# Performance work log

Hardware: AMD Instinct MI355X
Metric: run time of the kernel (lower is better)

## Reference

```python
import jax, jax.numpy as jnp
import numpy as np

N, E, C, H = 50000, 600000, 128, 8
Dh = C // H  # 16
LN_EPS = 1e-5


def _ln(x, g, b):
    mu = jnp.mean(x, axis=-1, keepdims=True)
    var = jnp.var(x, axis=-1, keepdims=True)
    return (x - mu) * jax.lax.rsqrt(var + LN_EPS) * g + b


def setup_inputs() -> dict:
    key = jax.random.key(0)
    ks = jax.random.split(key, 20)
    s = lambda d: 1.0 / np.sqrt(d)
    inp = {
        "node_feats": jax.random.normal(ks[0], (N, C), jnp.float32),
        "edge_feats": jax.random.normal(ks[1], (E, C), jnp.float32),
        "coords": jax.random.normal(ks[2], (N, 3), jnp.float32),
        "edge_index": jax.random.randint(ks[3], (2, E), 0, N, jnp.int64),
        # attention projections (no bias since in==out channels)
        "Wq": jax.random.normal(ks[4], (C, C), jnp.float32) * s(C),
        "Wk": jax.random.normal(ks[5], (C, C), jnp.float32) * s(C),
        "Wv": jax.random.normal(ks[6], (C, C), jnp.float32) * s(C),
        "We": jax.random.normal(ks[7], (C + 1, C), jnp.float32) * s(C + 1),
        # output projections (with bias)
        "Wo_n": jax.random.normal(ks[8], (C, C), jnp.float32) * s(C),
        "bo_n": jnp.zeros((C,), jnp.float32),
        "Wo_e": jax.random.normal(ks[9], (C, C), jnp.float32) * s(C),
        "bo_e": jnp.zeros((C,), jnp.float32),
        # layer norms
        "ln1n_g": jnp.ones((C,), jnp.float32), "ln1n_b": jnp.zeros((C,), jnp.float32),
        "ln1e_g": jnp.ones((C,), jnp.float32), "ln1e_b": jnp.zeros((C,), jnp.float32),
        "ln2n_g": jnp.ones((C,), jnp.float32), "ln2n_b": jnp.zeros((C,), jnp.float32),
        "ln2e_g": jnp.ones((C,), jnp.float32), "ln2e_b": jnp.zeros((C,), jnp.float32),
        # FFN MLPs (bias-free)
        "Wn1": jax.random.normal(ks[10], (C, 2 * C), jnp.float32) * s(C),
        "Wn2": jax.random.normal(ks[11], (2 * C, C), jnp.float32) * s(2 * C),
        "We1": jax.random.normal(ks[12], (C, 2 * C), jnp.float32) * s(C),
        "We2": jax.random.normal(ks[13], (2 * C, C), jnp.float32) * s(2 * C),
    }
    return inp


def reference(node_feats, edge_feats, coords, edge_index,
              Wq, Wk, Wv, We, Wo_n, bo_n, Wo_e, bo_e,
              ln1n_g, ln1n_b, ln1e_g, ln1e_b,
              ln2n_g, ln2n_b, ln2e_g, ln2e_b,
              Wn1, Wn2, We1, We2):
    row, col = edge_index[0], edge_index[1]
    h_in1, e_in1 = node_feats, edge_feats

    h = _ln(node_feats, ln1n_g, ln1n_b)
    e = _ln(edge_feats, ln1e_g, ln1e_b)

    q = (h @ Wq).reshape(N, H, Dh)
    k = (h @ Wk).reshape(N, H, Dh)
    v = (h @ Wv).reshape(N, H, Dh)

    # edge feature: concat with 0.1 * pairwise distance
    d = coords[row] - coords[col]                                  # [E,3]
    dist = 0.1 * jnp.sqrt(jnp.sum(d * d, axis=-1, keepdims=True))  # [E,1]
    ep = (jnp.concatenate([e, dist], axis=-1) @ We).reshape(E, H, Dh)

    alpha = jnp.clip(k[row] * q[col] / np.sqrt(Dh), -5.0, 5.0) * ep  # [E,H,Dh]
    alphax = jnp.exp(jnp.clip(jnp.sum(alpha, axis=-1, keepdims=True), -5.0, 5.0))  # [E,H,1]

    wV = jax.ops.segment_sum(v[row] * alphax, col, num_segments=N)  # [N,H,Dh]
    z = jax.ops.segment_sum(alphax, col, num_segments=N)            # [N,H,1]

    h_attn = (wV / (z + 1e-6)).reshape(N, C)
    e_attn = alpha.reshape(E, C)

    h2 = h_in1 + (h_attn @ Wo_n + bo_n)
    e2 = e_in1 + (e_attn @ Wo_e + bo_e)

    hn = _ln(h2, ln2n_g, ln2n_b)
    en = _ln(e2, ln2e_g, ln2e_b)

    h3 = jax.nn.silu(hn @ Wn1) @ Wn2
    e3 = jax.nn.silu(en @ We1) @ We2

    return (h2 + h3, e2 + e3)
```

## Files before the change

kernel.cpp:

```cpp
#include <hip/hip_runtime.h>
#include <math.h>

#define NN 50000
#define NE 600000
#define C 128
#define H 8
#define LN_EPS 1e-5f

typedef __attribute__((ext_vector_type(8))) short bf16x8;
typedef __attribute__((ext_vector_type(4))) float f32x4;
#define MFMA16 __builtin_amdgcn_mfma_f32_16x16x32_bf16

__device__ __forceinline__ float clip5(float x){ return fminf(fmaxf(x, -5.f), 5.f); }

__device__ __forceinline__ float red32(float v){
  v += __shfl_xor(v, 1);  v += __shfl_xor(v, 2);  v += __shfl_xor(v, 4);
  v += __shfl_xor(v, 8);  v += __shfl_xor(v, 16);
  return v;
}

__device__ __forceinline__ unsigned short f2bf(float f){
  union { float f; unsigned u; } c; c.f = f;
  unsigned r = (c.u + 0x7fffu + ((c.u >> 16) & 1u)) >> 16;
  return (unsigned short)r;
}
__device__ __forceinline__ float bf2f(unsigned short u){
  union { unsigned u; float f; } c; c.u = ((unsigned)u) << 16;
  return c.f;
}

__device__ __forceinline__ bf16x8 ld_frag(const unsigned short* p){
  return *(const bf16x8*)p;
}

__global__ void __launch_bounds__(256)
k_node_ln_qkv(const float* __restrict__ nf,
              const float* __restrict__ Wq, const float* __restrict__ Wk,
              const float* __restrict__ Wv,
              const float* __restrict__ g, const float* __restrict__ b,
              float* __restrict__ qb, float* __restrict__ kb, float* __restrict__ vb)
{
  __shared__ __align__(16) float s_h[8][C];
  const int tid = threadIdx.x;
  const int slot = tid >> 5, tg = tid & 31, c0 = tg * 4;
  const int node = blockIdx.x * 8 + slot;
  const bool valid = node < NN;
  const size_t nn = valid ? (size_t)node : 0;

  const float4 x = *(const float4*)(nf + nn * C + c0);
  float s  = x.x + x.y + x.z + x.w;
  float sq = x.x*x.x + x.y*x.y + x.z*x.z + x.w*x.w;
  s = red32(s); sq = red32(sq);
  const float mu   = s * (1.0f / C);
  const float rstd = rsqrtf(sq * (1.0f / C) - mu * mu + LN_EPS);
  const float4 gg = *(const float4*)(g + c0);
  const float4 bb = *(const float4*)(b + c0);
  float4 hv;
  hv.x = (x.x - mu) * rstd * gg.x + bb.x;
  hv.y = (x.y - mu) * rstd * gg.y + bb.y;
  hv.z = (x.z - mu) * rstd * gg.z + bb.z;
  hv.w = (x.w - mu) * rstd * gg.w + bb.w;
  *(float4*)&s_h[slot][c0] = hv;
  __syncthreads();

  const float4* Wq4 = (const float4*)Wq;
  const float4* Wk4 = (const float4*)Wk;
  const float4* Wv4 = (const float4*)Wv;
  float aq0=0,aq1=0,aq2=0,aq3=0, ak0=0,ak1=0,ak2=0,ak3=0, av0=0,av1=0,av2=0,av3=0;
  #pragma unroll 8
  for (int k = 0; k < C; ++k){
    const float h = s_h[slot][k];
    const float4 wq = Wq4[k*32 + tg];
    const float4 wk = Wk4[k*32 + tg];
    const float4 wv = Wv4[k*32 + tg];
    aq0 += h*wq.x; aq1 += h*wq.y; aq2 += h*wq.z; aq3 += h*wq.w;
    ak0 += h*wk.x; ak1 += h*wk.y; ak2 += h*wk.z; ak3 += h*wk.w;
    av0 += h*wv.x; av1 += h*wv.y; av2 += h*wv.z; av3 += h*wv.w;
  }
  if (valid){
    float4 o;
    o.x=aq0; o.y=aq1; o.z=aq2; o.w=aq3; *(float4*)(qb + nn*C + c0) = o;
    o.x=ak0; o.y=ak1; o.z=ak2; o.w=ak3; *(float4*)(kb + nn*C + c0) = o;
    o.x=av0; o.y=av1; o.z=av2; o.w=av3; *(float4*)(vb + nn*C + c0) = o;
  }
}

__global__ void k_zero(float* __restrict__ p, size_t n){
  size_t i = (size_t)blockIdx.x * blockDim.x + threadIdx.x;
  const size_t st = (size_t)gridDim.x * blockDim.x;
  for (; i < n; i += st) p[i] = 0.f;
}

__global__ void __launch_bounds__(256)
k_prep(const float* __restrict__ Wn1, const float* __restrict__ Wn2,
       const float* __restrict__ We1, const float* __restrict__ We2,
       const float* __restrict__ We,  const float* __restrict__ Woe,
       unsigned short* __restrict__ o,
       unsigned short* __restrict__ weTh, unsigned short* __restrict__ weTl,
       unsigned short* __restrict__ woeTh, unsigned short* __restrict__ woeTl,
       float* __restrict__ we128f)
{
  const int id = blockIdx.x * 256 + threadIdx.x;
  if (id < 131072){
    const int w = id >> 15, e = id & 32767;
    const float* src; int K, Nn;
    if      (w == 0){ src = Wn1; K = 128; Nn = 256; }
    else if (w == 1){ src = Wn2; K = 256; Nn = 128; }
    else if (w == 2){ src = We1; K = 128; Nn = 256; }
    else            { src = We2; K = 256; Nn = 128; }
    const int n = (K == 128) ? (e >> 7) : (e >> 8);
    const int k = e - n * K;
    const float v = src[(size_t)k * Nn + n];
    const unsigned short h = f2bf(v);
    const unsigned short l = f2bf(v - bf2f(h));
    unsigned short* oh = o + (size_t)w * 65536;
    oh[e] = h;
    oh[32768 + e] = l;
  } else if (id < 147456){
    const int e = id - 131072;
    const int n = e >> 7, k = e & 127;
    const float v = We[(size_t)k * 128 + n];
    const unsigned short h = f2bf(v);
    weTh[e] = h; weTl[e] = f2bf(v - bf2f(h));
  } else if (id < 163840){
    const int e = id - 147456;
    const int n = e >> 7, k = e & 127;
    const float v = Woe[(size_t)k * 128 + n];
    const unsigned short h = f2bf(v);
    woeTh[e] = h; woeTl[e] = f2bf(v - bf2f(h));
  } else if (id < 163968){
    const int c = id - 163840;
    we128f[c] = We[128 * 128 + c];
  }
}

__global__ void __launch_bounds__(256, 2)
k_edge_mfma(const float* __restrict__ ef, const float* __restrict__ coords,
            const int* __restrict__ eidx,
            const float* __restrict__ qb, const float* __restrict__ kb,
            const float* __restrict__ vb,
            const unsigned short* __restrict__ weTh, const unsigned short* __restrict__ weTl,
            const float* __restrict__ we128,
            const unsigned short* __restrict__ woeTh, const unsigned short* __restrict__ woeTl,
            const float* __restrict__ boe,
            const float* __restrict__ g1, const float* __restrict__ b1,
            const float* __restrict__ g2, const float* __restrict__ b2,
            float* __restrict__ wV, float* __restrict__ zz,
            float* __restrict__ e2_out,
            unsigned short* __restrict__ enh, unsigned short* __restrict__ enl)
{
  const int tid  = threadIdx.x;
  const int wid  = tid >> 6;
  const int lane = tid & 63;
  const int r = lane & 15, q = lane >> 4;
  const int ebase = (blockIdx.x * 4 + wid) * 16;
  const int edge  = ebase + r;
  const size_t e128 = (size_t)edge * 128;

  float xv[32];
  #pragma unroll
  for (int gk = 0; gk < 4; ++gk){
    const float4 a = *(const float4*)(ef + e128 + gk*32 + q*8);
    const float4 b = *(const float4*)(ef + e128 + gk*32 + q*8 + 4);
    xv[gk*8+0]=a.x; xv[gk*8+1]=a.y; xv[gk*8+2]=a.z; xv[gk*8+3]=a.w;
    xv[gk*8+4]=b.x; xv[gk*8+5]=b.y; xv[gk*8+6]=b.z; xv[gk*8+7]=b.w;
  }
  float s = 0.f, sq = 0.f;
  #pragma unroll
  for (int j = 0; j < 32; ++j){ s += xv[j]; sq += xv[j]*xv[j]; }
  s  += __shfl_xor(s, 16);  s  += __shfl_xor(s, 32);
  sq += __shfl_xor(sq, 16); sq += __shfl_xor(sq, 32);
  const float mu   = s * (1.f/128.f);
  const float rstd = rsqrtf(sq * (1.f/128.f) - mu*mu + LN_EPS);

  bf16x8 bhf[4], blf[4];
  #pragma unroll
  for (int gk = 0; gk < 4; ++gk){
    const float4 ga = *(const float4*)(g1 + gk*32 + q*8);
    const float4 gb = *(const float4*)(g1 + gk*32 + q*8 + 4);
    const float4 ba = *(const float4*)(b1 + gk*32 + q*8);
    const float4 bb = *(const float4*)(b1 + gk*32 + q*8 + 4);
    const float gv[8] = {ga.x,ga.y,ga.z,ga.w,gb.x,gb.y,gb.z,gb.w};
    const float bv[8] = {ba.x,ba.y,ba.z,ba.w,bb.x,bb.y,bb.z,bb.w};
    union { unsigned short u[8]; bf16x8 v; } ph, pl;
    #pragma unroll
    for (int j = 0; j < 8; ++j){
      const float e = (xv[gk*8+j] - mu) * rstd * gv[j] + bv[j];
      ph.u[j] = f2bf(e);
      pl.u[j] = f2bf(e - bf2f(ph.u[j]));
    }
    bhf[gk] = ph.v; blf[gk] = pl.v;
  }

  const int row = eidx[edge];
  const int col = eidx[NE + edge];
  float dist;
  {
    const size_t r3 = (size_t)row*3, c3 = (size_t)col*3;
    const float dx = coords[r3+0]-coords[c3+0];
    const float dy = coords[r3+1]-coords[c3+1];
    const float dz = coords[r3+2]-coords[c3+2];
    dist = 0.1f * sqrtf(dx*dx + dy*dy + dz*dz);
  }

  const int src0 = (r + ((lane & 16) << 1)) << 2;
  const int src1 = src0 + 64;
  const bool hisel = (lane >= 32);

  f32x4 acc[8];
  #pragma unroll
  for (int nt = 0; nt < 8; ++nt) acc[nt] = (f32x4){0.f,0.f,0.f,0.f};

  #pragma unroll
  for (int w4 = 0; w4 < 4; ++w4){
    int tw[2][4];
    #pragma unroll
    for (int t = 0; t < 2; ++t){
      const int p = 2*w4 + t;
      f32x4 c = (f32x4){0.f,0.f,0.f,0.f};
      const size_t abase = (size_t)(p*16 + r) * 128 + q*8;
      #pragma unroll
      for (int gk = 0; gk < 4; ++gk){
        const bf16x8 ah = ld_frag(weTh + abase + gk*32);
        const bf16x8 al = ld_frag(weTl + abase + gk*32);
        c = MFMA16(ah, bhf[gk], c, 0, 0, 0);
        c = MFMA16(ah, blf[gk], c, 0, 0, 0);
        c = MFMA16(al, bhf[gk], c, 0, 0, 0);
      }
      const float4 w128 = *(const float4*)(we128 + p*16 + q*4);
      const float4 kr   = *(const float4*)(kb + (size_t)row*128 + p*16 + q*4);
      const float4 qc   = *(const float4*)(qb + (size_t)col*128 + p*16 + q*4);
      float al4[4];
      al4[0] = clip5(kr.x*qc.x*0.25f) * (c[0] + dist*w128.x);
      al4[1] = clip5(kr.y*qc.y*0.25f) * (c[1] + dist*w128.y);
      al4[2] = clip5(kr.z*qc.z*0.25f) * (c[2] + dist*w128.z);
      al4[3] = clip5(kr.w*qc.w*0.25f) * (c[3] + dist*w128.w);

      float hs = al4[0]+al4[1]+al4[2]+al4[3];
      hs += __shfl_xor(hs, 16); hs += __shfl_xor(hs, 32);
      const float ax = expf(clip5(hs));

      const float4 vr = *(const float4*)(vb + (size_t)row*128 + p*16 + q*4);
      const size_t wb = (size_t)col*128 + p*16 + q*4;
      atomicAdd(&wV[wb+0], vr.x*ax);
      atomicAdd(&wV[wb+1], vr.y*ax);
      atomicAdd(&wV[wb+2], vr.z*ax);
      atomicAdd(&wV[wb+3], vr.w*ax);
      if (q == 0) atomicAdd(&zz[(size_t)col*H + p], ax);

      unsigned short th[4], tl[4];
      #pragma unroll
      for (int i = 0; i < 4; ++i){
        th[i] = f2bf(al4[i]);
        tl[i] = f2bf(al4[i] - bf2f(th[i]));
      }
      tw[t][0] = (int)th[0] | ((int)th[1] << 16);
      tw[t][1] = (int)th[2] | ((int)th[3] << 16);
      tw[t][2] = (int)tl[0] | ((int)tl[1] << 16);
      tw[t][3] = (int)tl[2] | ((int)tl[3] << 16);
    }

    union { int i[4]; bf16x8 v; } a2h, a2l;
    int u0, u1;
    u0 = __builtin_amdgcn_ds_bpermute(src0, tw[0][0]);
    u1 = __builtin_amdgcn_ds_bpermute(src0, tw[1][0]);
    a2h.i[0] = hisel ? u1 : u0;
    u0 = __builtin_amdgcn_ds_bpermute(src0, tw[0][1]);
    u1 = __builtin_amdgcn_ds_bpermute(src0, tw[1][1]);
    a2h.i[1] = hisel ? u1 : u0;
    u0 = __builtin_amdgcn_ds_bpermute(src1, tw[0][0]);
    u1 = __builtin_amdgcn_ds_bpermute(src1, tw[1][0]);
    a2h.i[2] = hisel ? u1 : u0;
    u0 = __builtin_amdgcn_ds_bpermute(src1, tw[0][1]);
    u1 = __builtin_amdgcn_ds_bpermute(src1, tw[1][1]);
    a2h.i[3] = hisel ? u1 : u0;
    u0 = __builtin_amdgcn_ds_bpermute(src0, tw[0][2]);
    u1 = __builtin_amdgcn_ds_bpermute(src0, tw[1][2]);
    a2l.i[0] = hisel ? u1 : u0;
    u0 = __builtin_amdgcn_ds_bpermute(src0, tw[0][3]);
    u1 = __builtin_amdgcn_ds_bpermute(src0, tw[1][3]);
    a2l.i[1] = hisel ? u1 : u0;
    u0 = __builtin_amdgcn_ds_bpermute(src1, tw[0][2]);
    u1 = __builtin_amdgcn_ds_bpermute(src1, tw[1][2]);
    a2l.i[2] = hisel ? u1 : u0;
    u0 = __builtin_amdgcn_ds_bpermute(src1, tw[0][3]);
    u1 = __builtin_amdgcn_ds_bpermute(src1, tw[1][3]);
    a2l.i[3] = hisel ? u1 : u0;

    #pragma unroll
    for (int nt = 0; nt < 8; ++nt){
      const size_t b2base = (size_t)(nt*16 + r)*128 + w4*32 + q*8;
      const bf16x8 b2h = ld_frag(woeTh + b2base);
      const bf16x8 b2l = ld_frag(woeTl + b2base);
      acc[nt] = MFMA16(a2h.v, b2h, acc[nt], 0, 0, 0);
      acc[nt] = MFMA16(a2l.v, b2h, acc[nt], 0, 0, 0);
      acc[nt] = MFMA16(a2h.v, b2l, acc[nt], 0, 0, 0);
    }
  }

  float boev[8], g2v[8], b2v[8];
  #pragma unroll
  for (int nt = 0; nt < 8; ++nt){
    boev[nt] = boe[nt*16 + r];
    g2v[nt]  = g2[nt*16 + r];
    b2v[nt]  = b2[nt*16 + r];
  }
  #pragma unroll
  for (int i = 0; i < 4; ++i){
    const int erow = ebase + q*4 + i;
    const size_t base = (size_t)erow * 128;
    float o[8];
    float s2 = 0.f, sq2 = 0.f;
    #pragma unroll
    for (int nt = 0; nt < 8; ++nt){
      o[nt] = acc[nt][i] + ef[base + nt*16 + r] + boev[nt];
      s2 += o[nt]; sq2 += o[nt]*o[nt];
    }
    s2  += __shfl_xor(s2, 1);  s2  += __shfl_xor(s2, 2);
    s2  += __shfl_xor(s2, 4);  s2  += __shfl_xor(s2, 8);
    sq2 += __shfl_xor(sq2, 1); sq2 += __shfl_xor(sq2, 2);
    sq2 += __shfl_xor(sq2, 4); sq2 += __shfl_xor(sq2, 8);
    const float mu2   = s2 * (1.f/128.f);
    const float rstd2 = rsqrtf(sq2 * (1.f/128.f) - mu2*mu2 + LN_EPS);
    #pragma unroll
    for (int nt = 0; nt < 8; ++nt){
      e2_out[base + nt*16 + r] = o[nt];
      const float en = (o[nt] - mu2)*rstd2*g2v[nt] + b2v[nt];
      const unsigned short h = f2bf(en);
      enh[base + nt*16 + r] = h;
      enl[base + nt*16 + r] = f2bf(en - bf2f(h));
    }
  }
}

__global__ void __launch_bounds__(256)
k_node_final(const float* __restrict__ nf, const float* __restrict__ wV,
             const float* __restrict__ zz,
             const float* __restrict__ Won, const float* __restrict__ bon,
             const float* __restrict__ g2, const float* __restrict__ b2,
             float* __restrict__ h2_out,
             unsigned short* __restrict__ hnh, unsigned short* __restrict__ hnl)
{
  __shared__ __align__(16) float sW[128*128];
  __shared__ __align__(16) float s_h[8][C];
  const int tid = threadIdx.x;
  {
    const float4* a = (const float4*)Won; float4* sa = (float4*)sW;
    for (int i = tid; i < 128*32; i += 256) sa[i] = a[i];
  }
  __syncthreads();
  const int slot = tid >> 5, tg = tid & 31, c0 = tg * 4;
  const float4* sW4 = (const float4*)sW;

  for (int n0 = blockIdx.x * 8; n0 < NN; n0 += gridDim.x * 8){
    const int node = n0 + slot;
    const bool valid = node < NN;
    const size_t nn = valid ? (size_t)node : 0;

    const float4 wv = *(const float4*)(wV + nn * C + c0);
    const float  zh = zz[nn * H + (c0 >> 4)] + 1e-6f;
    {
      float4 ha;
      ha.x = wv.x / zh; ha.y = wv.y / zh; ha.z = wv.z / zh; ha.w = wv.w / zh;
      *(float4*)&s_h[slot][c0] = ha;
    }
    __syncthreads();

    const float4 x  = *(const float4*)(nf + nn * C + c0);
    const float4 bo = *(const float4*)(bon + c0);
    float o0 = x.x + bo.x, o1 = x.y + bo.y, o2 = x.z + bo.z, o3 = x.w + bo.w;
    #pragma unroll 8
    for (int k = 0; k < C; ++k){
      const float hv = s_h[slot][k];
      const float4 w = sW4[k*32 + tg];
      o0 += hv*w.x; o1 += hv*w.y; o2 += hv*w.z; o3 += hv*w.w;
    }

    float s2  = o0 + o1 + o2 + o3;
    float sq2 = o0*o0 + o1*o1 + o2*o2 + o3*o3;
    s2 = red32(s2); sq2 = red32(sq2);
    const float mu2   = s2 * (1.0f / C);
    const float rstd2 = rsqrtf(sq2 * (1.0f / C) - mu2 * mu2 + LN_EPS);
    if (valid){
      float4 o; o.x=o0; o.y=o1; o.z=o2; o.w=o3;
      *(float4*)(h2_out + (size_t)node * C + c0) = o;
      const float4 gg = *(const float4*)(g2 + c0);
      const float4 bb = *(const float4*)(b2 + c0);
      float h0 = (o0 - mu2)*rstd2*gg.x + bb.x;
      float h1 = (o1 - mu2)*rstd2*gg.y + bb.y;
      float h2 = (o2 - mu2)*rstd2*gg.z + bb.z;
      float h3 = (o3 - mu2)*rstd2*gg.w + bb.w;
      ushort4 hh, ll;
      hh.x = f2bf(h0); ll.x = f2bf(h0 - bf2f(hh.x));
      hh.y = f2bf(h1); ll.y = f2bf(h1 - bf2f(hh.y));
      hh.z = f2bf(h2); ll.z = f2bf(h2 - bf2f(hh.z));
      hh.w = f2bf(h3); ll.w = f2bf(h3 - bf2f(hh.w));
      *(ushort4*)(hnh + (size_t)node * C + c0) = hh;
      *(ushort4*)(hnl + (size_t)node * C + c0) = ll;
    }
    __syncthreads();
  }
}

__global__ void __launch_bounds__(256, 2)
k_ffn_mfma(int M,
           const unsigned short* __restrict__ xh, const unsigned short* __restrict__ xl,
           const unsigned short* __restrict__ w1h, const unsigned short* __restrict__ w1l,
           const unsigned short* __restrict__ w2h, const unsigned short* __restrict__ w2l,
           float* __restrict__ out)
{
  const int tid  = threadIdx.x;
  const int wid  = tid >> 6;
  const int lane = tid & 63;
  const int r = lane & 15;
  const int q = lane >> 4;
  const int rowbase = (blockIdx.x * 4 + wid) * 32;

  bf16x8 bh[2][4], bl[2][4];
  #pragma unroll
  for (int s = 0; s < 2; ++s){
    int row = rowbase + s*16 + r;
    if (row > M-1) row = M-1;
    const size_t base = (size_t)row * 128 + q * 8;
    #pragma unroll
    for (int gk = 0; gk < 4; ++gk){
      bh[s][gk] = ld_frag(xh + base + gk*32);
      bl[s][gk] = ld_frag(xl + base + gk*32);
    }
  }

  f32x4 acc[2][8];
  #pragma unroll
  for (int s = 0; s < 2; ++s)
    #pragma unroll
    for (int nt = 0; nt < 8; ++nt)
      acc[s][nt] = (f32x4){0.f, 0.f, 0.f, 0.f};

  const int src0 = (r + ((lane & 16) << 1)) << 2;
  const int src1 = src0 + 64;
  const bool hi = (lane >= 32);

  for (int p = 0; p < 8; ++p){
    #pragma unroll
    for (int s = 0; s < 2; ++s){
      int tw[2][4];
      #pragma unroll
      for (int t = 0; t < 2; ++t){
        const size_t abase = (size_t)((2*p + t)*16 + r) * 128 + q*8;
        f32x4 c = (f32x4){0.f, 0.f, 0.f, 0.f};
        #pragma unroll
        for (int gk = 0; gk < 4; ++gk){
          bf16x8 ah = ld_frag(w1h + abase + gk*32);
          bf16x8 al = ld_frag(w1l + abase + gk*32);
          c = MFMA16(ah, bh[s][gk], c, 0, 0, 0);
          c = MFMA16(ah, bl[s][gk], c, 0, 0, 0);
          c = MFMA16(al, bh[s][gk], c, 0, 0, 0);
        }
        unsigned short th[4], tl_[4];
        #pragma unroll
        for (int i = 0; i < 4; ++i){
          float v = c[i];
          v = v / (1.f + __expf(-v));
          th[i]  = f2bf(v);
          tl_[i] = f2bf(v - bf2f(th[i]));
        }
        tw[t][0] = (int)th[0]  | ((int)th[1]  << 16);
        tw[t][1] = (int)th[2]  | ((int)th[3]  << 16);
        tw[t][2] = (int)tl_[0] | ((int)tl_[1] << 16);
        tw[t][3] = (int)tl_[2] | ((int)tl_[3] << 16);
      }
      int u0, u1;
      union { int i[4]; bf16x8 v; } a2h, a2l;
      u0 = __builtin_amdgcn_ds_bpermute(src0, tw[0][0]);
      u1 = __builtin_amdgcn_ds_bpermute(src0, tw[1][0]);
      a2h.i[0] = hi ? u1 : u0;
      u0 = __builtin_amdgcn_ds_bpermute(src0, tw[0][1]);
      u1 = __builtin_amdgcn_ds_bpermute(src0, tw[1][1]);
      a2h.i[1] = hi ? u1 : u0;
      u0 = __builtin_amdgcn_ds_bpermute(src1, tw[0][0]);
      u1 = __builtin_amdgcn_ds_bpermute(src1, tw[1][0]);
      a2h.i[2] = hi ? u1 : u0;
      u0 = __builtin_amdgcn_ds_bpermute(src1, tw[0][1]);
      u1 = __builtin_amdgcn_ds_bpermute(src1, tw[1][1]);
      a2h.i[3] = hi ? u1 : u0;
      u0 = __builtin_amdgcn_ds_bpermute(src0, tw[0][2]);
      u1 = __builtin_amdgcn_ds_bpermute(src0, tw[1][2]);
      a2l.i[0] = hi ? u1 : u0;
      u0 = __builtin_amdgcn_ds_bpermute(src0, tw[0][3]);
      u1 = __builtin_amdgcn_ds_bpermute(src0, tw[1][3]);
      a2l.i[1] = hi ? u1 : u0;
      u0 = __builtin_amdgcn_ds_bpermute(src1, tw[0][2]);
      u1 = __builtin_amdgcn_ds_bpermute(src1, tw[1][2]);
      a2l.i[2] = hi ? u1 : u0;
      u0 = __builtin_amdgcn_ds_bpermute(src1, tw[0][3]);
      u1 = __builtin_amdgcn_ds_bpermute(src1, tw[1][3]);
      a2l.i[3] = hi ? u1 : u0;

      #pragma unroll
      for (int nt = 0; nt < 8; ++nt){
        const size_t b2base = (size_t)(nt*16 + r) * 256 + p*32 + q*8;
        bf16x8 b2h = ld_frag(w2h + b2base);
        bf16x8 b2l = ld_frag(w2l + b2base);
        acc[s][nt] = MFMA16(a2h.v, b2h, acc[s][nt], 0, 0, 0);
        acc[s][nt] = MFMA16(a2l.v, b2h, acc[s][nt], 0, 0, 0);
        acc[s][nt] = MFMA16(a2h.v, b2l, acc[s][nt], 0, 0, 0);
      }
    }
  }

  #pragma unroll
  for (int s = 0; s < 2; ++s){
    #pragma unroll
    for (int nt = 0; nt < 8; ++nt){
      #pragma unroll
      for (int i = 0; i < 4; ++i){
        const int row = rowbase + s*16 + q*4 + i;
        if (row < M){
          const size_t idx = (size_t)row * 128 + nt*16 + r;
          out[idx] += acc[s][nt][i];
        }
      }
    }
  }
}

extern "C" void kernel_launch(void* const* d_in, const int* in_sizes, int n_in,
                              void* d_out, int out_size, void* d_ws, size_t ws_size,
                              hipStream_t stream)
{
  const float* nf     = (const float*)d_in[0];
  const float* ef     = (const float*)d_in[1];
  const float* coords = (const float*)d_in[2];
  const int*   eidx   = (const int*)  d_in[3];
  const float* Wq     = (const float*)d_in[4];
  const float* Wk     = (const float*)d_in[5];
  const float* Wv     = (const float*)d_in[6];
  const float* We     = (const float*)d_in[7];
  const float* Won    = (const float*)d_in[8];
  const float* bon    = (const float*)d_in[9];
  const float* Woe    = (const float*)d_in[10];
  const float* boe    = (const float*)d_in[11];
  const float* ln1ng  = (const float*)d_in[12];
  const float* ln1nb  = (const float*)d_in[13];
  const float* ln1eg  = (const float*)d_in[14];
  const float* ln1eb  = (const float*)d_in[15];
  const float* ln2ng  = (const float*)d_in[16];
  const float* ln2nb  = (const float*)d_in[17];
  const float* ln2eg  = (const float*)d_in[18];
  const float* ln2eb  = (const float*)d_in[19];
  const float* Wn1    = (const float*)d_in[20];
  const float* Wn2    = (const float*)d_in[21];
  const float* We1    = (const float*)d_in[22];
  const float* We2    = (const float*)d_in[23];

  float* out_h = (float*)d_out;
  float* out_e = out_h + (size_t)NN * C;

  float* ws = (float*)d_ws;
  float* qb = ws;
  float* kb = qb + (size_t)NN * C;
  float* vb = kb + (size_t)NN * C;
  float* wV = vb + (size_t)NN * C;
  float* zz = wV + (size_t)NN * C;
  unsigned short* hnh = (unsigned short*)(zz + (size_t)NN * H);
  unsigned short* hnl = hnh + (size_t)NN * C;
  unsigned short* enh = hnl + (size_t)NN * C;
  unsigned short* enl = enh + (size_t)NE * C;
  unsigned short* wts = enl + (size_t)NE * C;
  unsigned short* wn1h = wts + 0*32768;
  unsigned short* wn1l = wts + 1*32768;
  unsigned short* wn2h = wts + 2*32768;
  unsigned short* wn2l = wts + 3*32768;
  unsigned short* we1h = wts + 4*32768;
  unsigned short* we1l = wts + 5*32768;
  unsigned short* we2h = wts + 6*32768;
  unsigned short* we2l = wts + 7*32768;
  unsigned short* weTh  = wts + 8*32768;
  unsigned short* weTl  = weTh + 16384;
  unsigned short* woeTh = weTl + 16384;
  unsigned short* woeTl = woeTh + 16384;
  float*          we128 = (float*)(woeTl + 16384);

  hipLaunchKernelGGL(k_prep, dim3(641), dim3(256), 0, stream,
                     Wn1, Wn2, We1, We2, We, Woe,
                     wts, weTh, weTl, woeTh, woeTl, we128);
  hipLaunchKernelGGL(k_node_ln_qkv, dim3((NN + 7) / 8), dim3(256), 0, stream,
                     nf, Wq, Wk, Wv, ln1ng, ln1nb, qb, kb, vb);
  hipLaunchKernelGGL(k_zero, dim3(1024), dim3(256), 0, stream,
                     wV, (size_t)NN * C + (size_t)NN * H);
  hipLaunchKernelGGL(k_edge_mfma, dim3(NE / 64), dim3(256), 0, stream,
                     ef, coords, eidx, qb, kb, vb,
                     weTh, weTl, we128, woeTh, woeTl, boe,
                     ln1eg, ln1eb, ln2eg, ln2eb,
                     wV, zz, out_e, enh, enl);
  hipLaunchKernelGGL(k_node_final, dim3(1024), dim3(256), 0, stream,
                     nf, wV, zz, Won, bon, ln2ng, ln2nb, out_h, hnh, hnl);
  hipLaunchKernelGGL(k_ffn_mfma, dim3((NN + 127) / 128), dim3(256), 0, stream,
                     NN, hnh, hnl, wn1h, wn1l, wn2h, wn2l, out_h);
  hipLaunchKernelGGL(k_ffn_mfma, dim3((NE + 127) / 128), dim3(256), 0, stream,
                     NE, enh, enl, we1h, we1l, we2h, we2l, out_e);
}
```

Measured before the change: 3.200 ms.

## Replace scatter atomics with CSR build and per-node gather aggregation

Builds a CSR index of edges grouped by destination node: count, three-pass scan and fill, with one atomic per edge. The edge kernel now stores only per-edge exp weights, and a new gather kernel gives each node one wavefront that sums v[row]*alpha and z without float atomics. This removes about 77M float atomicAdds on wV and zz, and makes the summation order deterministic. The cost is several extra kernel launches, an irregular gather over the CSR, and the axbuf written into the hnh region, which must not be overwritten before the gather reads it.

New measurement: 2.771 ms. -13.4%, faster.

```diff
diff --git a/kernel.cpp b/kernel.cpp
--- a/kernel.cpp
+++ b/kernel.cpp
@@ -6,6 +6,7 @@
 #define C 128
 #define H 8
 #define LN_EPS 1e-5f
+#define NB1 196
 
 typedef __attribute__((ext_vector_type(8))) short bf16x8;
 typedef __attribute__((ext_vector_type(4))) float f32x4;
@@ -134,18 +135,104 @@
   }
 }
 
+__global__ void __launch_bounds__(256)
+k_count(const int* __restrict__ eidx, int* __restrict__ deg){
+  const int e = blockIdx.x * 256 + threadIdx.x;
+  if (e < NE) atomicAdd(&deg[eidx[NE + e]], 1);
+}
+
+__global__ void __launch_bounds__(256)
+k_scan1(const int* __restrict__ deg, int* __restrict__ ex, int* __restrict__ bsum){
+  __shared__ int sd[256];
+  const int i = threadIdx.x;
+  const int t = blockIdx.x * 256 + i;
+  const int v = (t < NN) ? deg[t] : 0;
+  sd[i] = v;
+  __syncthreads();
+  for (int off = 1; off < 256; off <<= 1){
+    const int add = (i >= off) ? sd[i - off] : 0;
+    __syncthreads();
+    sd[i] += add;
+    __syncthreads();
+  }
+  if (t < NN) ex[t] = sd[i] - v;
+  if (i == 255) bsum[blockIdx.x] = sd[255];
+}
+
+__global__ void __launch_bounds__(256)
+k_scan2(const int* __restrict__ bsum, int* __restrict__ bpre){
+  __shared__ int sd[256];
+  const int i = threadIdx.x;
+  const int v = (i < NB1) ? bsum[i] : 0;
+  sd[i] = v;
+  __syncthreads();
+  for (int off = 1; off < 256; off <<= 1){
+    const int add = (i >= off) ? sd[i - off] : 0;
+    __syncthreads();
+    sd[i] += add;
+    __syncthreads();
+  }
+  if (i < NB1) bpre[i] = sd[i] - v;
+}
+
+__global__ void __launch_bounds__(256)
+k_scan3(const int* __restrict__ ex, const int* __restrict__ bpre,
+        int* __restrict__ rowptr, int* __restrict__ cursor){
+  const int t = blockIdx.x * 256 + threadIdx.x;
+  if (t < NN){
+    const int r = ex[t] + bpre[t >> 8];
+    rowptr[t] = r;
+    cursor[t] = r;
+    if (t == 0) rowptr[NN] = NE;
+  }
+}
+
+__global__ void __launch_bounds__(256)
+k_fill(const int* __restrict__ eidx, int* __restrict__ cursor, int* __restrict__ csr){
+  const int e = blockIdx.x * 256 + threadIdx.x;
+  if (e < NE){
+    const int col = eidx[NE + e];
+    const int pos = atomicAdd(&cursor[col], 1);
+    csr[pos] = e;
+  }
+}
+
+__global__ void __launch_bounds__(256)
+k_gather(const int* __restrict__ rowptr, const int* __restrict__ csr,
+         const int* __restrict__ eidx, const float* __restrict__ vb,
+         const float* __restrict__ axbuf,
+         float* __restrict__ wV, float* __restrict__ zz)
+{
+  const int wid = threadIdx.x >> 6, lane = threadIdx.x & 63;
+  const int n = blockIdx.x * 4 + wid;
+  if (n >= NN) return;
+  const int s = rowptr[n], t = rowptr[n + 1];
+  const int c0 = lane * 2, h = lane >> 3;
+  float a0 = 0.f, a1 = 0.f, zacc = 0.f;
+  for (int p = s; p < t; ++p){
+    const int eid = csr[p];
+    const int row = eidx[eid];
+    const float ax = axbuf[(size_t)eid * 8 + h];
+    const float2 vv = *(const float2*)(vb + (size_t)row * 128 + c0);
+    a0 += vv.x * ax; a1 += vv.y * ax;
+    if (lane < 8) zacc += axbuf[(size_t)eid * 8 + lane];
+  }
+  wV[(size_t)n * 128 + c0]     = a0;
+  wV[(size_t)n * 128 + c0 + 1] = a1;
+  if (lane < 8) zz[(size_t)n * 8 + lane] = zacc;
+}
+
 __global__ void __launch_bounds__(256, 2)
 k_edge_mfma(const float* __restrict__ ef, const float* __restrict__ coords,
             const int* __restrict__ eidx,
             const float* __restrict__ qb, const float* __restrict__ kb,
-            const float* __restrict__ vb,
             const unsigned short* __restrict__ weTh, const unsigned short* __restrict__ weTl,
             const float* __restrict__ we128,
             const unsigned short* __restrict__ woeTh, const unsigned short* __restrict__ woeTl,
             const float* __restrict__ boe,
             const float* __restrict__ g1, const float* __restrict__ b1,
             const float* __restrict__ g2, const float* __restrict__ b2,
-            float* __restrict__ wV, float* __restrict__ zz,
+            float* __restrict__ axbuf,
             float* __restrict__ e2_out,
             unsigned short* __restrict__ enh, unsigned short* __restrict__ enl)
 {
@@ -240,13 +327,7 @@
       hs += __shfl_xor(hs, 16); hs += __shfl_xor(hs, 32);
       const float ax = expf(clip5(hs));
 
-      const float4 vr = *(const float4*)(vb + (size_t)row*128 + p*16 + q*4);
-      const size_t wb = (size_t)col*128 + p*16 + q*4;
-      atomicAdd(&wV[wb+0], vr.x*ax);
-      atomicAdd(&wV[wb+1], vr.y*ax);
-      atomicAdd(&wV[wb+2], vr.z*ax);
-      atomicAdd(&wV[wb+3], vr.w*ax);
-      if (q == 0) atomicAdd(&zz[(size_t)col*H + p], ax);
+      if (q == 0) axbuf[(size_t)edge * 8 + p] = ax;
 
       unsigned short th[4], tl[4];
       #pragma unroll
@@ -580,19 +661,38 @@
   unsigned short* woeTh = weTl + 16384;
   unsigned short* woeTl = woeTh + 16384;
   float*          we128 = (float*)(woeTl + 16384);
+  int* ideg  = (int*)(we128 + 128);
+  int* itmp  = ideg + NN;
+  int* ibsum = itmp + NN;
+  int* ibpre = ibsum + 256;
+  int* irowp = ibpre + 256;
+  int* icsr  = irowp + NN + 1;
+  float* axbuf = (float*)hnh;
 
   hipLaunchKernelGGL(k_prep, dim3(641), dim3(256), 0, stream,
                      Wn1, Wn2, We1, We2, We, Woe,
                      wts, weTh, weTl, woeTh, woeTl, we128);
   hipLaunchKernelGGL(k_node_ln_qkv, dim3((NN + 7) / 8), dim3(256), 0, stream,
                      nf, Wq, Wk, Wv, ln1ng, ln1nb, qb, kb, vb);
-  hipLaunchKernelGGL(k_zero, dim3(1024), dim3(256), 0, stream,
-                     wV, (size_t)NN * C + (size_t)NN * H);
+  hipLaunchKernelGGL(k_zero, dim3(196), dim3(256), 0, stream,
+                     (float*)ideg, (size_t)NN);
+  hipLaunchKernelGGL(k_count, dim3((NE + 255) / 256), dim3(256), 0, stream,
+                     eidx, ideg);
+  hipLaunchKernelGGL(k_scan1, dim3(NB1), dim3(256), 0, stream,
+                     ideg, itmp, ibsum);
+  hipLaunchKernelGGL(k_scan2, dim3(1), dim3(256), 0, stream,
+                     ibsum, ibpre);
+  hipLaunchKernelGGL(k_scan3, dim3(NB1), dim3(256), 0, stream,
+                     itmp, ibpre, irowp, ideg);
+  hipLaunchKernelGGL(k_fill, dim3((NE + 255) / 256), dim3(256), 0, stream,
+                     eidx, ideg, icsr);
   hipLaunchKernelGGL(k_edge_mfma, dim3(NE / 64), dim3(256), 0, stream,
-                     ef, coords, eidx, qb, kb, vb,
+                     ef, coords, eidx, qb, kb,
                      weTh, weTl, we128, woeTh, woeTl, boe,
                      ln1eg, ln1eb, ln2eg, ln2eb,
-                     wV, zz, out_e, enh, enl);
+                     axbuf, out_e, enh, enl);
+  hipLaunchKernelGGL(k_gather, dim3((NN + 3) / 4), dim3(256), 0, stream,
+                     irowp, icsr, eidx, vb, axbuf, wV, zz);
   hipLaunchKernelGGL(k_node_final, dim3(1024), dim3(256), 0, stream,
                      nf, wV, zz, Won, bon, ln2ng, ln2nb, out_h, hnh, hnl);
   hipLaunchKernelGGL(k_ffn_mfma, dim3((NN + 127) / 128), dim3(256), 0, stream,
```
